# Kernel tuning notes

Hardware: AMD Instinct MI355X
Metric: run time of the kernel (lower is better)

The kernel has to match this reference:

```python
import jax, jax.numpy as jnp
import numpy as np

B, L, D_MODEL = 2, 2048, 1024
N_HEAD, D_K, D_V = 16, 64, 64


def setup_inputs() -> dict:
    key = jax.random.key(0)
    ks = jax.random.split(key, 11)
    s = lambda fan_in: 1.0 / np.sqrt(fan_in)
    return {
        "q": jax.random.normal(ks[0], (B, L, D_MODEL), dtype=jnp.float32),
        "k": jax.random.normal(ks[1], (B, L, D_MODEL), dtype=jnp.float32),
        "v": jax.random.normal(ks[2], (B, L, D_MODEL), dtype=jnp.float32),
        "Wq": jax.random.uniform(ks[3], (D_MODEL, N_HEAD * D_K), jnp.float32, -s(D_MODEL), s(D_MODEL)),
        "bq": jax.random.uniform(ks[4], (N_HEAD * D_K,), jnp.float32, -s(D_MODEL), s(D_MODEL)),
        "Wk": jax.random.uniform(ks[5], (D_MODEL, N_HEAD * D_K), jnp.float32, -s(D_MODEL), s(D_MODEL)),
        "bk": jax.random.uniform(ks[6], (N_HEAD * D_K,), jnp.float32, -s(D_MODEL), s(D_MODEL)),
        "Wv": jax.random.uniform(ks[7], (D_MODEL, N_HEAD * D_V), jnp.float32, -s(D_MODEL), s(D_MODEL)),
        "bv": jax.random.uniform(ks[8], (N_HEAD * D_V,), jnp.float32, -s(D_MODEL), s(D_MODEL)),
        "Wo": jax.random.uniform(ks[9], (N_HEAD * D_V, D_MODEL), jnp.float32, -s(N_HEAD * D_V), s(N_HEAD * D_V)),
        "bo": jax.random.uniform(ks[10], (D_MODEL,), jnp.float32, -s(N_HEAD * D_V), s(N_HEAD * D_V)),
    }


def reference(q, k, v, Wq, bq, Wk, bk, Wv, bv, Wo, bo):
    b, lq, _ = q.shape
    lk = k.shape[1]
    # QKV projections then split heads: [B, H, L, Dk]
    qh = (q @ Wq + bq).reshape(b, lq, N_HEAD, D_K).transpose(0, 2, 1, 3)
    kh = (k @ Wk + bk).reshape(b, lk, N_HEAD, D_K).transpose(0, 2, 1, 3)
    vh = (v @ Wv + bv).reshape(b, lk, N_HEAD, D_V).transpose(0, 2, 1, 3)
    # naive SDPA: materialize [B, H, Lq, Lk] scores, scale by sqrt(d_k)
    scores = jnp.einsum("bhqd,bhkd->bhqk", qh, kh) / jnp.sqrt(jnp.float32(D_K))
    attn = jax.nn.softmax(scores, axis=-1)
    out = jnp.einsum("bhqk,bhkd->bhqd", attn, vh)
    # merge heads and output projection (dropout = identity in eval)
    out = out.transpose(0, 2, 1, 3).reshape(b, lq, N_HEAD * D_V)
    out = out @ Wo + bo
    return out, attn
```

## Files before the change

kernel.cpp:

```cpp
#include <hip/hip_runtime.h>
#include <hip/hip_bf16.h>

typedef float f32x4 __attribute__((ext_vector_type(4)));
typedef short bf16x8 __attribute__((ext_vector_type(8)));

#define MFMA_BF16 __builtin_amdgcn_mfma_f32_16x16x32_bf16

static __device__ __forceinline__ unsigned short f2bf(float f) {
    __hip_bfloat16 h = __float2bfloat16(f);
    return __builtin_bit_cast(unsigned short, h);
}
static __device__ __forceinline__ unsigned int pack2(float a, float b) {
    return (unsigned int)f2bf(a) | ((unsigned int)f2bf(b) << 16);
}

static __device__ __forceinline__ void gl16(const unsigned short* g, unsigned short* l) {
    unsigned short* gg = const_cast<unsigned short*>(g);
    __builtin_amdgcn_global_load_lds(
        (__attribute__((address_space(1))) unsigned int*)gg,
        (__attribute__((address_space(3))) unsigned int*)l, 16, 0, 0);
}

__global__ __launch_bounds__(256) void conv_wT(
    const float* __restrict__ Wq, const float* __restrict__ Wk,
    const float* __restrict__ Wv, const float* __restrict__ Wo,
    unsigned short* __restrict__ WT)
{
    const int z = blockIdx.z;
    const float* W = (z == 0) ? Wq : (z == 1) ? Wk : (z == 2) ? Wv : Wo;
    unsigned short* Wt = WT + (size_t)z * 1048576;
    const int k0 = blockIdx.x * 64, n0 = blockIdx.y * 64;
    __shared__ float tl[64][68];
    const int t = threadIdx.x;
    const int r = t >> 2, cs = (t & 3) * 16;
#pragma unroll
    for (int j = 0; j < 4; j++)
        *(float4*)&tl[r][cs + j * 4] = *(const float4*)&W[(size_t)(k0 + r) * 1024 + n0 + cs + j * 4];
    __syncthreads();
    const int n = t & 63, kb = (t >> 6) * 16;
#pragma unroll
    for (int j = 0; j < 4; j++) {
        const int kk = kb + j * 4;
        uint2 o = { pack2(tl[kk][n], tl[kk + 1][n]), pack2(tl[kk + 2][n], tl[kk + 3][n]) };
        *(uint2*)&Wt[(size_t)(n0 + n) * 1024 + k0 + kk] = o;
    }
}

__global__ __launch_bounds__(256) void conv_bf16(
    const float* __restrict__ q, const float* __restrict__ k, const float* __restrict__ v,
    unsigned short* __restrict__ qkvb)
{
    const int z = blockIdx.y;
    const float* s = (z == 0) ? q : (z == 1) ? k : v;
    unsigned short* d = qkvb + (size_t)z * 4194304;
    const size_t i = ((size_t)blockIdx.x * 256 + threadIdx.x) * 8;
    float4 a = *(const float4*)&s[i], b = *(const float4*)&s[i + 4];
    uint4 o = { pack2(a.x, a.y), pack2(a.z, a.w), pack2(b.x, b.y), pack2(b.z, b.w) };
    *(uint4*)&d[i] = o;
}

static __device__ __forceinline__ void gemm_core(
    const unsigned short* __restrict__ A, const unsigned short* __restrict__ Bt,
    unsigned short* lA, unsigned short* lB, int m0, int n0, f32x4 (&acc)[4][4])
{
    const int t = threadIdx.x;
    const int w = t >> 6, lane = t & 63, lrow = lane & 15, lkg = lane >> 4;
    const int wr = w >> 1, wc = w & 1;
    const int srow = lane >> 2, sseg = (lane & 3) * 8;

    for (int k0 = 0; k0 < 1024; k0 += 32) {
        gl16(&A[(size_t)(m0 + w * 32 + srow) * 1024 + k0 + sseg], &lA[w * 1024]);
        gl16(&A[(size_t)(m0 + w * 32 + 16 + srow) * 1024 + k0 + sseg], &lA[w * 1024 + 512]);
        gl16(&Bt[(size_t)(n0 + w * 32 + srow) * 1024 + k0 + sseg], &lB[w * 1024]);
        gl16(&Bt[(size_t)(n0 + w * 32 + 16 + srow) * 1024 + k0 + sseg], &lB[w * 1024 + 512]);
        __syncthreads();
        bf16x8 af[4], bfr[4];
#pragma unroll
        for (int mi = 0; mi < 4; mi++)
            af[mi] = *(const bf16x8*)&lA[(wr * 64 + mi * 16 + lrow) * 32 + lkg * 8];
#pragma unroll
        for (int ni = 0; ni < 4; ni++)
            bfr[ni] = *(const bf16x8*)&lB[(wc * 64 + ni * 16 + lrow) * 32 + lkg * 8];
#pragma unroll
        for (int mi = 0; mi < 4; mi++)
#pragma unroll
            for (int ni = 0; ni < 4; ni++)
                acc[mi][ni] = MFMA_BF16(af[mi], bfr[ni], acc[mi][ni], 0, 0, 0);
        __syncthreads();
    }
}

__global__ __launch_bounds__(256) void gemm_qkv(
    const unsigned short* __restrict__ qkvb, const unsigned short* __restrict__ WT,
    const float* __restrict__ bq, const float* __restrict__ bk, const float* __restrict__ bv,
    unsigned short* __restrict__ Qh, unsigned short* __restrict__ Kh, unsigned short* __restrict__ Vt)
{
    const int z = blockIdx.z;
    const unsigned short* A = qkvb + (size_t)z * 4194304;
    const unsigned short* Bt = WT + (size_t)z * 1048576;
    const float* bias = (z == 0) ? bq : (z == 1) ? bk : bv;

    const int n0 = blockIdx.x * 128, m0 = blockIdx.y * 128;
    __shared__ unsigned short lA[4096], lB[4096];
    f32x4 acc[4][4];
#pragma unroll
    for (int i = 0; i < 4; i++)
#pragma unroll
        for (int j = 0; j < 4; j++) acc[i][j] = (f32x4){0.f, 0.f, 0.f, 0.f};

    gemm_core(A, Bt, lA, lB, m0, n0, acc);

    const int t = threadIdx.x;
    const int w = t >> 6, lane = t & 63, lrow = lane & 15, lkg = lane >> 4;
    const int wr = w >> 1, wc = w & 1;

#pragma unroll
    for (int mi = 0; mi < 4; mi++) {
#pragma unroll
        for (int ni = 0; ni < 4; ni++) {
            const int gn = n0 + wc * 64 + ni * 16 + lrow;
            const float bb = bias[gn];
            const int hh = gn >> 6, dk = gn & 63;
            const int gm0 = m0 + wr * 64 + mi * 16 + lkg * 4;
            const int b2 = gm0 >> 11, ll = gm0 & 2047;
            if (z < 2) {
                unsigned short* C = (z == 0) ? Qh : Kh;
#pragma unroll
                for (int r = 0; r < 4; r++)
                    C[(size_t)((b2 * 16 + hh) * 2048 + ll + r) * 64 + dk] = f2bf(acc[mi][ni][r] + bb);
            } else {
                uint2 o = { pack2(acc[mi][ni][0] + bb, acc[mi][ni][1] + bb),
                            pack2(acc[mi][ni][2] + bb, acc[mi][ni][3] + bb) };
                *(uint2*)&Vt[(size_t)((b2 * 16 + hh) * 64 + dk) * 2048 + ll] = o;
            }
        }
    }
}

__global__ __launch_bounds__(256) void gemm_o(
    const unsigned short* __restrict__ Oh, const unsigned short* __restrict__ WoT,
    const float* __restrict__ bo, float* __restrict__ out)
{
    const int n0 = blockIdx.x * 128, m0 = blockIdx.y * 128;
    __shared__ unsigned short lA[4096], lB[4096];
    f32x4 acc[4][4];
#pragma unroll
    for (int i = 0; i < 4; i++)
#pragma unroll
        for (int j = 0; j < 4; j++) acc[i][j] = (f32x4){0.f, 0.f, 0.f, 0.f};

    gemm_core(Oh, WoT, lA, lB, m0, n0, acc);

    const int t = threadIdx.x;
    const int w = t >> 6, lane = t & 63, lrow = lane & 15, lkg = lane >> 4;
    const int wr = w >> 1, wc = w & 1;

#pragma unroll
    for (int mi = 0; mi < 4; mi++) {
#pragma unroll
        for (int ni = 0; ni < 4; ni++) {
            const int gn = n0 + wc * 64 + ni * 16 + lrow;
            const float bb = bo[gn];
            const int gm0 = m0 + wr * 64 + mi * 16 + lkg * 4;
#pragma unroll
            for (int r = 0; r < 4; r++)
                out[(size_t)(gm0 + r) * 1024 + gn] = acc[mi][ni][r] + bb;
        }
    }
}

__global__ __launch_bounds__(512, 4) void attn_kernel(
    const unsigned short* __restrict__ Qh, const unsigned short* __restrict__ Kh,
    const unsigned short* __restrict__ Vt, float* __restrict__ attn,
    unsigned short* __restrict__ Oh)
{
    const int bid = blockIdx.x;
    const int swz = (bid & 7) * 64 + (bid >> 3);
    const int bh = swz >> 4;
    const int q0 = (swz & 15) * 128;
    const int b = bh >> 4, h = bh & 15;
    const int t = threadIdx.x;
    const int w = t >> 6, lane = t & 63, ql = lane & 15, kg = lane >> 4;

    __shared__ unsigned short lS[2][8192];
    __shared__ float stg[8][1024];

    const size_t kvbase = (size_t)bh * 2048 * 64;
    const float C = 0.18033688011112042f;

    const unsigned short* qptr = Qh + kvbase + (size_t)(q0 + w * 16 + ql) * 64 + kg * 8;
    const bf16x8 qf0 = *(const bf16x8*)(qptr);
    const bf16x8 qf1 = *(const bf16x8*)(qptr + 32);

    const unsigned short* Kbh = Kh + kvbase;
    const unsigned short* Vbh = Vt + kvbase;

    const int kr = w * 8 + (lane >> 3);
    const int kc = (lane & 7) ^ (kr & 7);
    const int r7 = ql & 7;

    f32x4 ls4 = (f32x4){0.f, 0.f, 0.f, 0.f};
    {
        gl16(Kbh + (size_t)kr * 64 + kc * 8, &lS[0][w * 512]);
        gl16(Kbh + (size_t)(kr + 64) * 64 + kc * 8, &lS[0][4096 + w * 512]);
        __syncthreads();
        for (int kt = 0; kt < 16; ++kt) {
            const int c = kt & 1;
            if (kt < 15) {
                const int k0n = (kt + 1) * 128;
                gl16(Kbh + (size_t)(k0n + kr) * 64 + kc * 8, &lS[c ^ 1][w * 512]);
                gl16(Kbh + (size_t)(k0n + kr + 64) * 64 + kc * 8, &lS[c ^ 1][4096 + w * 512]);
            } else {
                gl16(Kbh + (size_t)kr * 64 + kc * 8, &lS[0][w * 512]);
                gl16(Vbh + (size_t)kr * 2048 + kc * 8, &lS[0][4096 + w * 512]);
            }
            const unsigned short* Kl = lS[c];
            f32x4 sacc[8];
            __builtin_amdgcn_s_setprio(1);
#pragma unroll
            for (int ni = 0; ni < 8; ni++) {
                const int rb = (ni * 16 + ql) * 64;
                bf16x8 kf0 = *(const bf16x8*)&Kl[rb + ((kg ^ r7) * 8)];
                bf16x8 kf1 = *(const bf16x8*)&Kl[rb + (((4 + kg) ^ r7) * 8)];
                f32x4 s = (f32x4){0.f, 0.f, 0.f, 0.f};
                s = MFMA_BF16(kf0, qf0, s, 0, 0, 0);
                sacc[ni] = MFMA_BF16(kf1, qf1, s, 0, 0, 0);
            }
            __builtin_amdgcn_s_setprio(0);
#pragma unroll
            for (int ni = 0; ni < 8; ni++)
#pragma unroll
                for (int r = 0; r < 4; r++) ls4[r] += exp2f(sacc[ni][r] * C);
            __syncthreads();
        }
    }
    float lsum = ls4[0] + ls4[1] + ls4[2] + ls4[3];
    lsum += __shfl_xor(lsum, 16);
    lsum += __shfl_xor(lsum, 32);
    const float mlg = -log2f(lsum);

    f32x4 acco[4];
#pragma unroll
    for (int nv = 0; nv < 4; nv++) acco[nv] = (f32x4){0.f, 0.f, 0.f, 0.f};

    float* abase = attn + ((size_t)bh * 2048 + q0 + w * 16) * 2048 + ql * 4;

    for (int kt = 0; kt < 32; ++kt) {
        const int c = kt & 1;
        if (kt < 31) {
            const int k0n = (kt + 1) * 64;
            gl16(Kbh + (size_t)(k0n + kr) * 64 + kc * 8, &lS[c ^ 1][w * 512]);
            gl16(Vbh + (size_t)kr * 2048 + k0n + kc * 8, &lS[c ^ 1][4096 + w * 512]);
        }
        const int k0 = kt * 64;
        const unsigned short* Kl = lS[c];
        const unsigned short* Vl = &lS[c][4096];

        f32x4 sacc[4];
        __builtin_amdgcn_s_setprio(1);
#pragma unroll
        for (int ni = 0; ni < 4; ni++) {
            const int rb = (ni * 16 + ql) * 64;
            bf16x8 kf0 = *(const bf16x8*)&Kl[rb + ((kg ^ r7) * 8)];
            bf16x8 kf1 = *(const bf16x8*)&Kl[rb + (((4 + kg) ^ r7) * 8)];
            f32x4 s = (f32x4){0.f, 0.f, 0.f, 0.f};
            s = MFMA_BF16(kf0, qf0, s, 0, 0, 0);
            sacc[ni] = MFMA_BF16(kf1, qf1, s, 0, 0, 0);
        }
        __builtin_amdgcn_s_setprio(0);

#pragma unroll
        for (int ni = 0; ni < 4; ni++) {
            f32x4 p;
#pragma unroll
            for (int r = 0; r < 4; r++) p[r] = exp2f(fmaf(sacc[ni][r], C, mlg));
            *(f32x4*)&stg[w][ql * 64 + ni * 16 + kg * 4] = p;
        }

        __builtin_amdgcn_s_setprio(1);
#pragma unroll
        for (int s4 = 0; s4 < 2; s4++) {
            const float* ps = &stg[w][ql * 64 + s4 * 32 + kg * 8];
            f32x4 pa = *(const f32x4*)ps;
            f32x4 pb = *(const f32x4*)(ps + 4);
            uint4 pw = { pack2(pa[0], pa[1]), pack2(pa[2], pa[3]),
                         pack2(pb[0], pb[1]), pack2(pb[2], pb[3]) };
            bf16x8 pf = __builtin_bit_cast(bf16x8, pw);
#pragma unroll
            for (int nv = 0; nv < 4; nv++) {
                const int cc = (s4 * 4 + kg) ^ r7;
                bf16x8 vf = *(const bf16x8*)&Vl[(nv * 16 + ql) * 64 + cc * 8];
                acco[nv] = MFMA_BF16(vf, pf, acco[nv], 0, 0, 0);
            }
        }
        __builtin_amdgcn_s_setprio(0);

#pragma unroll
        for (int i = 0; i < 4; i++) {
            const int row = i * 4 + kg;
            f32x4 vv = *(const f32x4*)&stg[w][row * 64 + ql * 4];
            __builtin_nontemporal_store(vv, (f32x4*)&abase[(size_t)row * 2048 + k0]);
        }
        __syncthreads();
    }

    unsigned short* obase = Oh + ((size_t)(b * 2048 + q0 + w * 16 + ql)) * 1024 + h * 64 + kg * 4;
#pragma unroll
    for (int nv = 0; nv < 4; nv++) {
        uint2 o2 = { pack2(acco[nv][0], acco[nv][1]), pack2(acco[nv][2], acco[nv][3]) };
        *(uint2*)&obase[nv * 16] = o2;
    }
}

extern "C" void kernel_launch(void* const* d_in, const int* in_sizes, int n_in,
                              void* d_out, int out_size, void* d_ws, size_t ws_size,
                              hipStream_t stream) {
    const float* q  = (const float*)d_in[0];
    const float* k  = (const float*)d_in[1];
    const float* v  = (const float*)d_in[2];
    const float* Wq = (const float*)d_in[3];
    const float* bq = (const float*)d_in[4];
    const float* Wk = (const float*)d_in[5];
    const float* bk = (const float*)d_in[6];
    const float* Wv = (const float*)d_in[7];
    const float* bv = (const float*)d_in[8];
    const float* Wo = (const float*)d_in[9];
    const float* bo = (const float*)d_in[10];

    float* out  = (float*)d_out;
    float* attn = out + (size_t)2 * 2048 * 1024;

    const size_t HS = 4194304;
    unsigned short* qkvb = (unsigned short*)d_ws;
    unsigned short* WT   = qkvb + 3 * HS;
    unsigned short* Qh   = WT + 4 * 1048576;
    unsigned short* Kh   = Qh + HS;
    unsigned short* Vt   = Kh + HS;
    unsigned short* Oh   = Vt + HS;

    conv_wT  <<<dim3(16, 16, 4), 256, 0, stream>>>(Wq, Wk, Wv, Wo, WT);
    conv_bf16<<<dim3(2048, 3),  256, 0, stream>>>(q, k, v, qkvb);
    gemm_qkv <<<dim3(8, 32, 3), 256, 0, stream>>>(qkvb, WT, bq, bk, bv, Qh, Kh, Vt);
    attn_kernel<<<dim3(512), 512, 0, stream>>>(Qh, Kh, Vt, attn, Oh);
    gemm_o   <<<dim3(8, 32),   256, 0, stream>>>(Oh, WT + 3 * 1048576, bo, out);
}
```

Before: 268.2 us.

## Triple-buffer GEMM LDS loads with async prefetch and remap blocks per XCD

The shared GEMM core moves from a single-buffered load/sync/compute loop to a three-stage LDS ring. Async global-to-LDS loads are issued two tiles ahead, and explicit vmcnt waits replace the two __syncthreads per iteration. MFMA sections get raised wave priority. Both GEMM kernels now launch a 1D grid whose block index is remapped so that consecutive tiles land on the same XCD for better L2 reuse. This triples LDS use per block, which may lower occupancy, and the hand-counted waitcnt is a correctness risk.

```diff
diff --git a/kernel.cpp b/kernel.cpp
--- a/kernel.cpp
+++ b/kernel.cpp
@@ -68,26 +68,55 @@
     const int wr = w >> 1, wc = w & 1;
     const int srow = lane >> 2, sseg = (lane & 3) * 8;
 
-    for (int k0 = 0; k0 < 1024; k0 += 32) {
-        gl16(&A[(size_t)(m0 + w * 32 + srow) * 1024 + k0 + sseg], &lA[w * 1024]);
-        gl16(&A[(size_t)(m0 + w * 32 + 16 + srow) * 1024 + k0 + sseg], &lA[w * 1024 + 512]);
-        gl16(&Bt[(size_t)(n0 + w * 32 + srow) * 1024 + k0 + sseg], &lB[w * 1024]);
-        gl16(&Bt[(size_t)(n0 + w * 32 + 16 + srow) * 1024 + k0 + sseg], &lB[w * 1024 + 512]);
-        __syncthreads();
+    const unsigned short* Ab0 = &A[(size_t)(m0 + w * 32 + srow) * 1024 + sseg];
+    const unsigned short* Ab1 = &A[(size_t)(m0 + w * 32 + 16 + srow) * 1024 + sseg];
+    const unsigned short* Bb0 = &Bt[(size_t)(n0 + w * 32 + srow) * 1024 + sseg];
+    const unsigned short* Bb1 = &Bt[(size_t)(n0 + w * 32 + 16 + srow) * 1024 + sseg];
+
+#define GISSUE(tt, buf)                                     \
+    do {                                                    \
+        const int k0_ = (tt) * 32;                          \
+        gl16(Ab0 + k0_, &lA[(buf) * 4096 + w * 1024]);      \
+        gl16(Ab1 + k0_, &lA[(buf) * 4096 + w * 1024 + 512]);\
+        gl16(Bb0 + k0_, &lB[(buf) * 4096 + w * 1024]);      \
+        gl16(Bb1 + k0_, &lB[(buf) * 4096 + w * 1024 + 512]);\
+    } while (0)
+
+    GISSUE(0, 0);
+    GISSUE(1, 1);
+    __builtin_amdgcn_sched_barrier(0);
+
+    int bcur = 0;
+    for (int tt = 0; tt < 32; ++tt) {
+        if (tt < 31) { asm volatile("s_waitcnt vmcnt(4)" ::: "memory"); }
+        else         { asm volatile("s_waitcnt vmcnt(0)" ::: "memory"); }
+        __builtin_amdgcn_s_barrier();
+        __builtin_amdgcn_sched_barrier(0);
+        if (tt + 2 < 32) {
+            int bpre = bcur + 2; if (bpre >= 3) bpre -= 3;
+            GISSUE(tt + 2, bpre);
+        }
+        __builtin_amdgcn_sched_barrier(0);
+
+        const unsigned short* la = &lA[bcur * 4096];
+        const unsigned short* lb = &lB[bcur * 4096];
         bf16x8 af[4], bfr[4];
 #pragma unroll
         for (int mi = 0; mi < 4; mi++)
-            af[mi] = *(const bf16x8*)&lA[(wr * 64 + mi * 16 + lrow) * 32 + lkg * 8];
+            af[mi] = *(const bf16x8*)&la[(wr * 64 + mi * 16 + lrow) * 32 + lkg * 8];
 #pragma unroll
         for (int ni = 0; ni < 4; ni++)
-            bfr[ni] = *(const bf16x8*)&lB[(wc * 64 + ni * 16 + lrow) * 32 + lkg * 8];
+            bfr[ni] = *(const bf16x8*)&lb[(wc * 64 + ni * 16 + lrow) * 32 + lkg * 8];
+        __builtin_amdgcn_s_setprio(1);
 #pragma unroll
         for (int mi = 0; mi < 4; mi++)
 #pragma unroll
             for (int ni = 0; ni < 4; ni++)
                 acc[mi][ni] = MFMA_BF16(af[mi], bfr[ni], acc[mi][ni], 0, 0, 0);
-        __syncthreads();
-    }
+        __builtin_amdgcn_s_setprio(0);
+        bcur = (bcur == 2) ? 0 : bcur + 1;
+    }
+#undef GISSUE
 }
 
 __global__ __launch_bounds__(256) void gemm_qkv(
@@ -95,13 +124,16 @@
     const float* __restrict__ bq, const float* __restrict__ bk, const float* __restrict__ bv,
     unsigned short* __restrict__ Qh, unsigned short* __restrict__ Kh, unsigned short* __restrict__ Vt)
 {
-    const int z = blockIdx.z;
+    const int u0 = blockIdx.x;
+    const int u = (u0 & 7) * 96 + (u0 >> 3);
+    const int z = u >> 8, rm = u & 255;
+    const int m0 = ((rm >> 3) & 31) * 128, n0 = (rm & 7) * 128;
+
     const unsigned short* A = qkvb + (size_t)z * 4194304;
     const unsigned short* Bt = WT + (size_t)z * 1048576;
     const float* bias = (z == 0) ? bq : (z == 1) ? bk : bv;
 
-    const int n0 = blockIdx.x * 128, m0 = blockIdx.y * 128;
-    __shared__ unsigned short lA[4096], lB[4096];
+    __shared__ unsigned short lA[3 * 4096], lB[3 * 4096];
     f32x4 acc[4][4];
 #pragma unroll
     for (int i = 0; i < 4; i++)
@@ -141,8 +173,11 @@
     const unsigned short* __restrict__ Oh, const unsigned short* __restrict__ WoT,
     const float* __restrict__ bo, float* __restrict__ out)
 {
-    const int n0 = blockIdx.x * 128, m0 = blockIdx.y * 128;
-    __shared__ unsigned short lA[4096], lB[4096];
+    const int u0 = blockIdx.x;
+    const int u = (u0 & 7) * 32 + (u0 >> 3);
+    const int m0 = (u >> 3) * 128, n0 = (u & 7) * 128;
+
+    __shared__ unsigned short lA[3 * 4096], lB[3 * 4096];
     f32x4 acc[4][4];
 #pragma unroll
     for (int i = 0; i < 4; i++)
@@ -340,7 +375,7 @@
 
     conv_wT  <<<dim3(16, 16, 4), 256, 0, stream>>>(Wq, Wk, Wv, Wo, WT);
     conv_bf16<<<dim3(2048, 3),  256, 0, stream>>>(q, k, v, qkvb);
-    gemm_qkv <<<dim3(8, 32, 3), 256, 0, stream>>>(qkvb, WT, bq, bk, bv, Qh, Kh, Vt);
+    gemm_qkv <<<dim3(768), 256, 0, stream>>>(qkvb, WT, bq, bk, bv, Qh, Kh, Vt);
     attn_kernel<<<dim3(512), 512, 0, stream>>>(Qh, Kh, Vt, attn, Oh);
-    gemm_o   <<<dim3(8, 32),   256, 0, stream>>>(Oh, WT + 3 * 1048576, bo, out);
-}
+    gemm_o   <<<dim3(256), 256, 0, stream>>>(Oh, WT + 3 * 1048576, bo, out);
+}
```

Result: faster. 248.8 us (-7.2%).
